# Performance work log

Hardware: AMD Instinct MI355X
Metric: run time of the kernel (lower is better)

## Reference

```python
import jax, jax.numpy as jnp
import numpy as np
import math

N_ROW, N_COL, MID_DIM = 16, 16, 256
B, S, D, K, N_NEURONS = 4, 4096, 1024, 8, 64


def setup_inputs() -> dict:
    key = jax.random.key(0)
    ks = jax.random.split(key, 8)
    return {
        "x": jax.random.normal(ks[0], (B, S, D), dtype=jnp.float32),
        "neuron_idx": jax.random.randint(ks[1], (B, S, K), 0, N_NEURONS),
        "neuron_weights": jax.random.uniform(ks[2], (B, S, K), dtype=jnp.float32),
        "neuron_recipe": jax.random.normal(ks[3], (N_NEURONS, N_ROW * N_COL), dtype=jnp.float32) * 0.02,
        "row_basis": jax.random.normal(ks[4], (N_ROW, D, MID_DIM), dtype=jnp.float32) * 0.02,
        "col_basis": jax.random.normal(ks[5], (N_COL, MID_DIM, D), dtype=jnp.float32) * 0.02,
        "out_w": jax.random.normal(ks[6], (D, D), dtype=jnp.float32) * 0.02,
        "out_b": jnp.zeros((D,), dtype=jnp.float32),
        "alpha": jnp.asarray(0.1, dtype=jnp.float32),
    }


def reference(x, neuron_idx, neuron_weights, neuron_recipe, row_basis, col_basis, out_w, out_b, alpha):
    Bx, Sx, Dx = x.shape
    # --- recipe routing: gather per-token recipes, softmax, weighted sum ---
    sel = neuron_recipe[neuron_idx]                     # [B,S,k,RC]
    sel = jax.nn.softmax(sel, axis=-1)
    token_recipe = jnp.sum(sel * neuron_weights[..., None], axis=2)  # [B,S,RC]
    recipe = jax.nn.softmax(token_recipe, axis=-1).reshape(Bx, Sx, N_ROW, N_COL)
    row_w = recipe.sum(axis=-1)                         # [B,S,n_row]
    col_w = recipe.sum(axis=-2)                         # [B,S,n_col]
    # --- dynamic Q/K: sum over basis middle/last axis commutes with contraction ---
    q = jnp.einsum('bsr,rm->bsm', row_w, row_basis.sum(axis=1))  # [B,S,mid]
    kk = jnp.einsum('bsc,cm->bsm', col_w, col_basis.sum(axis=2)) # [B,S,mid]
    scores = jnp.einsum('bsm,btm->bst', q, kk) / math.sqrt(MID_DIM)  # [B,S,S]
    causal = jnp.triu(jnp.ones((Sx, Sx), dtype=bool), k=1)
    scores = jnp.where(causal, -jnp.inf, scores)
    attn = jax.nn.softmax(scores, axis=-1)
    context = jnp.einsum('bst,btd->bsd', attn, x)        # [B,S,D]
    transform = jnp.einsum('bsc,cd->bsd', col_w, col_basis.sum(axis=1))  # [B,S,D]
    out = jax.nn.gelu(context + alpha * transform, approximate=False)
    return out @ out_w.T + out_b
```

## Files before the change

### kernel.cpp

```cpp
#include <hip/hip_runtime.h>
#include <hip/hip_bf16.h>
#include <math.h>

#define BB 4
#define SS 4096
#define DDIM 1024
#define KSEL 8
#define NR 16
#define NC 16
#define MID 256
#define RC 256
#define TOK (BB*SS)

typedef __hip_bfloat16 bf16;
typedef short short8 __attribute__((ext_vector_type(8)));
typedef short short4v __attribute__((ext_vector_type(4)));
typedef float floatx4 __attribute__((ext_vector_type(4)));
typedef float floatx16 __attribute__((ext_vector_type(16)));
#define MFMA16(a,b,c) __builtin_amdgcn_mfma_f32_16x16x32_bf16(a,b,c,0,0,0)
#define MFMA32(a,b,c) __builtin_amdgcn_mfma_f32_32x32x16_bf16(a,b,c,0,0,0)

__device__ __forceinline__ float uihf(unsigned v) { union { unsigned i; float f; } t; t.i = v; return t.f; }
__device__ __forceinline__ float b2f(bf16 h) { return __bfloat162float(h); }
__device__ __forceinline__ float bs2f(short s) { return uihf(((unsigned)(unsigned short)s) << 16); }
__device__ __forceinline__ short f2bs(float f) {
    bf16 h = __float2bfloat16(f);
    return *reinterpret_cast<short*>(&h);
}
__device__ __forceinline__ float loadf(const void* p, size_t i, bool f32m) {
    return f32m ? ((const float*)p)[i] : b2f(((const bf16*)p)[i]);
}

#define WS_RB   16
#define WS_CB2  4112
#define WS_CB1  8208
#define WS_CW   24592
#define WS_BIAS 286736
#define WS_QK   287760
#define WS_WB   4482064
#define WS_XT   5006352
#define WS_LV   13394960

struct DetectArgs { const void* p[9]; int n[9]; };

__global__ void k_detect(DetectArgs A, int* __restrict__ flags) {
    int b = blockIdx.x;
    int tid = threadIdx.x;
    if (b == 9) {
        float* w = (float*)flags;
        for (int i = tid; i < 24576; i += 256) w[WS_RB + i] = 0.f;
        return;
    }
    const unsigned short* u = (const unsigned short*)A.p[b];
    int n = A.n[b]; if (n > 4096) n = 4096;
    float m = 0.f;
    for (int i = tid; i < n; i += 256) {
        unsigned v = (((unsigned)u[i]) << 16) & 0x7fffffffu;
        float f = uihf(v);
        if (f == f) m = fmaxf(m, f);
    }
    for (int o = 32; o; o >>= 1) m = fmaxf(m, __shfl_xor(m, o));
    __shared__ float red[4];
    if ((tid & 63) == 0) red[tid >> 6] = m;
    __syncthreads();
    if (tid == 0) {
        float mm = fmaxf(fmaxf(red[0], red[1]), fmaxf(red[2], red[3]));
        flags[b] = (b == 1) ? 0 : (mm > 1e4f ? 1 : 0);
    }
}

__global__ void k_rbsum(const void* __restrict__ rb, float* __restrict__ ws) {
    bool f32m = ((const int*)ws)[4] != 0;
    int r = blockIdx.x >> 3, dc = blockIdx.x & 7, m = threadIdx.x;
    size_t base = (size_t)r*DDIM*MID + (size_t)dc*128*MID + m;
    float s = 0.f;
    #pragma unroll 8
    for (int d = 0; d < 128; ++d) s += loadf(rb, base + (size_t)d*MID, f32m);
    atomicAdd(&ws[WS_RB + r*MID + m], s);
}

__global__ void k_cb2(const void* __restrict__ cb, float* __restrict__ ws) {
    bool f32m = ((const int*)ws)[5] != 0;
    int row = blockIdx.x*4 + (threadIdx.x >> 6);
    int lane = threadIdx.x & 63;
    size_t base = (size_t)row*DDIM;
    float s = 0.f;
    for (int i = lane; i < DDIM; i += 64) s += loadf(cb, base + i, f32m);
    for (int o = 32; o; o >>= 1) s += __shfl_down(s, o);
    if (lane == 0) ws[WS_CB2 + row] = s;
}

__global__ void k_cb1(const void* __restrict__ cb, float* __restrict__ ws) {
    bool f32m = ((const int*)ws)[5] != 0;
    int c = blockIdx.x >> 4;
    int d = (((blockIdx.x >> 2) & 3) << 8) + threadIdx.x;
    int m0 = (blockIdx.x & 3) * 64;
    size_t base = (size_t)c*MID*DDIM + (size_t)m0*DDIM + d;
    float s = 0.f;
    #pragma unroll 8
    for (int m = 0; m < 64; ++m) s += loadf(cb, base + (size_t)m*DDIM, f32m);
    atomicAdd(&ws[WS_CB1 + c*DDIM + d], s);
}

__global__ void k_wcvt(const void* __restrict__ w, const void* __restrict__ bias,
                       float* __restrict__ ws) {
    bool wf32 = ((const int*)ws)[6] != 0, bf32 = ((const int*)ws)[7] != 0;
    short* Wb = (short*)(ws + WS_WB);
    float* biasf = ws + WS_BIAS;
    int bx = blockIdx.x, tid = threadIdx.x;
    if (bx == 512) {
        for (int i = tid; i < DDIM; i += 256) biasf[i] = loadf(bias, i, bf32);
        return;
    }
    size_t base = (size_t)bx*2048 + tid*8;
    if (wf32) {
        const float* s = (const float*)w + base;
        float4 a = *(const float4*)s, c = *(const float4*)(s + 4);
        short8 v;
        v[0]=f2bs(a.x); v[1]=f2bs(a.y); v[2]=f2bs(a.z); v[3]=f2bs(a.w);
        v[4]=f2bs(c.x); v[5]=f2bs(c.y); v[6]=f2bs(c.z); v[7]=f2bs(c.w);
        *(short8*)(Wb + base) = v;
    } else {
        *(uint4*)(Wb + base) = *(const uint4*)((const short*)w + base);
    }
}

__global__ void k_xt(const void* __restrict__ x, float* __restrict__ ws) {
    bool xf32 = ((const int*)ws)[0] != 0;
    __shared__ short T[64][72];
    int tid = threadIdx.x;
    int s0 = blockIdx.x*64, d0 = blockIdx.y*64, b = blockIdx.z;
    int rr = tid >> 4, c4 = (tid & 15)*4;
    #pragma unroll
    for (int it = 0; it < 4; ++it) {
        int r = rr + it*16;
        size_t off = (size_t)(b*SS + s0 + r)*DDIM + d0 + c4;
        float v[4];
        if (xf32) {
            float4 a = *(const float4*)((const float*)x + off);
            v[0]=a.x; v[1]=a.y; v[2]=a.z; v[3]=a.w;
        } else {
            const short* p = (const short*)x + off;
            #pragma unroll
            for (int j = 0; j < 4; ++j) v[j] = bs2f(p[j]);
        }
        #pragma unroll
        for (int j = 0; j < 4; ++j) T[c4+j][r] = f2bs(v[j]);
    }
    __syncthreads();
    int dr = tid >> 2, sc = (tid & 3)*16;
    short8 u0 = *(const short8*)(&T[dr][sc]);
    short8 u1 = *(const short8*)(&T[dr][sc+8]);
    short* dst = (short*)(ws + WS_XT) + ((size_t)(b*DDIM + d0 + dr))*SS + s0 + sc;
    *(short8*)dst = u0;
    *(short8*)(dst + 8) = u1;
}

__global__ __launch_bounds__(256) void k_route(const int* __restrict__ nidx,
        const void* __restrict__ nw, const void* __restrict__ rmat,
        float* __restrict__ ws) {
    const bool f2 = ((const int*)ws)[2] != 0, f3 = ((const int*)ws)[3] != 0;
    const int lane = threadIdx.x & 63;
    const int tok = blockIdx.x*4 + (threadIdx.x >> 6);

    int idx8 = 0; float w8 = 0.f;
    if (lane < KSEL) {
        idx8 = nidx[tok*KSEL + lane];
        w8   = loadf(nw, tok*KSEL + lane, f2);
    }

    float acc[4] = {0.f,0.f,0.f,0.f};
    #pragma unroll 1
    for (int k = 0; k < KSEL; ++k) {
        int   id_k = __shfl(idx8, k);
        float wk   = __shfl(w8, k);
        float v[4];
        if (f3) {
            float4 t = *(const float4*)((const float*)rmat + (size_t)id_k*RC + lane*4);
            v[0]=t.x; v[1]=t.y; v[2]=t.z; v[3]=t.w;
        } else {
            short4v t = *(const short4v*)((const short*)rmat + (size_t)id_k*RC + lane*4);
            #pragma unroll
            for (int j = 0; j < 4; ++j) v[j] = bs2f(t[j]);
        }
        float m = fmaxf(fmaxf(v[0],v[1]), fmaxf(v[2],v[3]));
        #pragma unroll
        for (int o = 32; o; o >>= 1) m = fmaxf(m, __shfl_xor(m, o));
        float e[4], s = 0.f;
        #pragma unroll
        for (int j = 0; j < 4; ++j) { e[j] = __expf(v[j]-m); s += e[j]; }
        #pragma unroll
        for (int o = 32; o; o >>= 1) s += __shfl_xor(s, o);
        float r = wk / s;
        #pragma unroll
        for (int j = 0; j < 4; ++j) acc[j] += r * e[j];
    }
    {
        float m = fmaxf(fmaxf(acc[0],acc[1]), fmaxf(acc[2],acc[3]));
        #pragma unroll
        for (int o = 32; o; o >>= 1) m = fmaxf(m, __shfl_xor(m, o));
        float s = 0.f;
        #pragma unroll
        for (int j = 0; j < 4; ++j) { acc[j] = __expf(acc[j]-m); s += acc[j]; }
        #pragma unroll
        for (int o = 32; o; o >>= 1) s += __shfl_xor(s, o);
        float inv = 1.f / s;
        #pragma unroll
        for (int j = 0; j < 4; ++j) acc[j] *= inv;
    }
    float rwp = acc[0]+acc[1]+acc[2]+acc[3];
    rwp += __shfl_xor(rwp, 1); rwp += __shfl_xor(rwp, 2);
    float cw4[4] = {acc[0],acc[1],acc[2],acc[3]};
    #pragma unroll
    for (int j = 0; j < 4; ++j) {
        cw4[j] += __shfl_xor(cw4[j], 4);
        cw4[j] += __shfl_xor(cw4[j], 8);
        cw4[j] += __shfl_xor(cw4[j], 16);
        cw4[j] += __shfl_xor(cw4[j], 32);
    }
    if (lane < 4) {
        float4 t; t.x=cw4[0]; t.y=cw4[1]; t.z=cw4[2]; t.w=cw4[3];
        *(float4*)(ws + WS_CW + (size_t)tok*NC + lane*4) = t;
    }
    float rwAll[NR], cwAll[NC];
    #pragma unroll
    for (int r = 0; r < NR; ++r) rwAll[r] = __shfl(rwp, r*4);
    #pragma unroll
    for (int c = 0; c < NC; ++c) cwAll[c] = __shfl(cw4[c & 3], c >> 2);
    float qv[4] = {0.f,0.f,0.f,0.f}, kv[4] = {0.f,0.f,0.f,0.f};
    #pragma unroll
    for (int r = 0; r < NR; ++r) {
        float4 t = *(const float4*)(ws + WS_RB + r*MID + lane*4);
        qv[0] += rwAll[r]*t.x; qv[1] += rwAll[r]*t.y;
        qv[2] += rwAll[r]*t.z; qv[3] += rwAll[r]*t.w;
    }
    #pragma unroll
    for (int c = 0; c < NC; ++c) {
        float4 t = *(const float4*)(ws + WS_CB2 + c*MID + lane*4);
        kv[0] += cwAll[c]*t.x; kv[1] += cwAll[c]*t.y;
        kv[2] += cwAll[c]*t.z; kv[3] += cwAll[c]*t.w;
    }
    short* Qh  = (short*)(ws + WS_QK);
    short* KKh = Qh + (size_t)TOK*MID;
    short4v qo, ko;
    #pragma unroll
    for (int j = 0; j < 4; ++j) { qo[j] = f2bs(qv[j]*0.0625f); ko[j] = f2bs(kv[j]); }
    *(short4v*)(Qh  + (size_t)tok*MID + lane*4) = qo;
    *(short4v*)(KKh + (size_t)tok*MID + lane*4) = ko;
}

__global__ __launch_bounds__(256) void k_att(const float* __restrict__ ws,
        float* __restrict__ U, const void* __restrict__ alphap) {
    __shared__ __align__(16) short Ks[32*264];
    __shared__ __align__(16) short Ps[64*40];
    __shared__ __align__(16) short cb1T[512*40];
    __shared__ __align__(16) short cwsb[64*40];
    __shared__ float lv[64];
    const int tid = threadIdx.x;
    const int w = tid >> 6, lane = tid & 63, lq = lane & 15, quad = lane >> 4;
    const int bx = blockIdx.x;
    const int g = bx & 7;
    const int d0 = (g & 1)*512, b = g >> 1;
    const int qt = 63 - (bx >> 3);
    const int q0 = qt*64;
    const int ntiles = 2*qt + 2;
    const bool af32 = ((const int*)ws)[8] != 0;
    const short* Qh  = (const short*)(ws + WS_QK);
    const short* KKh = Qh + (size_t)TOK*MID;
    const short* xT  = (const short*)(ws + WS_XT);

    {
        for (int r = tid; r < 512; r += 256) {
            const float* src = ws + WS_CB1 + d0 + r;
            short* dst = cb1T + r*40;
            #pragma unroll
            for (int c = 0; c < 16; ++c) dst[c] = f2bs(src[c*DDIM]);
            #pragma unroll
            for (int c = 16; c < 32; ++c) dst[c] = 0;
        }
    }
    {
        int r = tid >> 2, c4 = (tid & 3)*4;
        const float* cwp = ws + WS_CW + (size_t)(b*SS + q0 + r)*NC + c4;
        short* dst = cwsb + r*40;
        #pragma unroll
        for (int j = 0; j < 4; ++j) dst[c4 + j] = f2bs(cwp[j]);
        #pragma unroll
        for (int j = 0; j < 4; ++j) dst[16 + c4 + j] = 0;
    }
    const int rsw = (lq >> 2) & 3;
    const short* pa_rd = Ps + lq*40 + ((quad ^ rsw) << 3);
    short* pd_base = Ps + (w*16 + quad*4)*40 + (lq & 7);
    const int kr = tid >> 3, ksg = (tid & 7)*32;
    short* kdst = Ks + kr*264 + ksg;
    float alpha = af32 ? ((const float*)alphap)[0] : bs2f(((const short*)alphap)[0]);

    short8 qa[8];
    {
        const short* qrow = Qh + (size_t)(b*SS + q0 + w*16 + lq)*MID + quad*8;
        #pragma unroll
        for (int ks = 0; ks < 8; ++ks) qa[ks] = *(const short8*)(qrow + ks*32);
    }
    floatx4 acc[4][8];
    #pragma unroll
    for (int qi = 0; qi < 4; ++qi)
        #pragma unroll
        for (int di = 0; di < 8; ++di) acc[qi][di] = (floatx4){0.f,0.f,0.f,0.f};
    float l[4] = {0.f,0.f,0.f,0.f};

    const short* xb_base = xT + (size_t)(b*DDIM + d0 + w*128 + lq)*SS + quad*8;
    const short* ksrc0 = KKh + (size_t)(b*SS + kr)*MID + ksg;
    short8 kp0 = *(const short8*)(ksrc0);
    short8 kp1 = *(const short8*)(ksrc0 + 8);
    short8 kp2 = *(const short8*)(ksrc0 + 16);
    short8 kp3 = *(const short8*)(ksrc0 + 24);

    #pragma unroll 1
    for (int it = 0; it < ntiles; ++it) {
        const int t0 = it*32;
        *(short8*)(kdst)      = kp0;
        *(short8*)(kdst + 8)  = kp1;
        *(short8*)(kdst + 16) = kp2;
        *(short8*)(kdst + 24) = kp3;
        if (it + 1 < ntiles) {
            const short* ks_n = ksrc0 + (size_t)(it + 1)*32*MID;
            kp0 = *(const short8*)(ks_n);
            kp1 = *(const short8*)(ks_n + 8);
            kp2 = *(const short8*)(ks_n + 16);
            kp3 = *(const short8*)(ks_n + 24);
        }
        const short* xx = xb_base + it*32;
        short8 xf0 = *(const short8*)(xx);
        short8 xf1 = *(const short8*)(xx + (size_t)16*SS);
        short8 xf2 = *(const short8*)(xx + (size_t)32*SS);
        short8 xf3 = *(const short8*)(xx + (size_t)48*SS);
        short8 xf4 = *(const short8*)(xx + (size_t)64*SS);
        short8 xf5 = *(const short8*)(xx + (size_t)80*SS);
        short8 xf6 = *(const short8*)(xx + (size_t)96*SS);
        short8 xf7 = *(const short8*)(xx + (size_t)112*SS);
        __syncthreads();
        #pragma unroll
        for (int h = 0; h < 2; ++h) {
            floatx4 s = (floatx4){0.f,0.f,0.f,0.f};
            const short* kb = Ks + (h*16 + lq)*264 + quad*8;
            #pragma unroll
            for (int ks = 0; ks < 8; ++ks)
                s = MFMA16(qa[ks], *(const short8*)(kb + ks*32), s);
            int t = t0 + h*16 + lq;
            int qg = q0 + w*16 + quad*4;
            short* pd = pd_base + (((h*2 + (lq >> 3)) ^ quad) << 3);
            #pragma unroll
            for (int r = 0; r < 4; ++r) {
                float p = (t <= qg + r) ? __expf(s[r]) : 0.f;
                l[r] += p;
                pd[r*40] = f2bs(p);
            }
        }
        __syncthreads();
        {
            short8 pa0 = *(const short8*)(pa_rd);
            short8 pa1 = *(const short8*)(pa_rd + 16*40);
            short8 pa2 = *(const short8*)(pa_rd + 32*40);
            short8 pa3 = *(const short8*)(pa_rd + 48*40);
            acc[0][0] = MFMA16(pa0, xf0, acc[0][0]);
            acc[1][0] = MFMA16(pa1, xf0, acc[1][0]);
            acc[2][0] = MFMA16(pa2, xf0, acc[2][0]);
            acc[3][0] = MFMA16(pa3, xf0, acc[3][0]);
            acc[0][1] = MFMA16(pa0, xf1, acc[0][1]);
            acc[1][1] = MFMA16(pa1, xf1, acc[1][1]);
            acc[2][1] = MFMA16(pa2, xf1, acc[2][1]);
            acc[3][1] = MFMA16(pa3, xf1, acc[3][1]);
            acc[0][2] = MFMA16(pa0, xf2, acc[0][2]);
            acc[1][2] = MFMA16(pa1, xf2, acc[1][2]);
            acc[2][2] = MFMA16(pa2, xf2, acc[2][2]);
            acc[3][2] = MFMA16(pa3, xf2, acc[3][2]);
            acc[0][3] = MFMA16(pa0, xf3, acc[0][3]);
            acc[1][3] = MFMA16(pa1, xf3, acc[1][3]);
            acc[2][3] = MFMA16(pa2, xf3, acc[2][3]);
            acc[3][3] = MFMA16(pa3, xf3, acc[3][3]);
            acc[0][4] = MFMA16(pa0, xf4, acc[0][4]);
            acc[1][4] = MFMA16(pa1, xf4, acc[1][4]);
            acc[2][4] = MFMA16(pa2, xf4, acc[2][4]);
            acc[3][4] = MFMA16(pa3, xf4, acc[3][4]);
            acc[0][5] = MFMA16(pa0, xf5, acc[0][5]);
            acc[1][5] = MFMA16(pa1, xf5, acc[1][5]);
            acc[2][5] = MFMA16(pa2, xf5, acc[2][5]);
            acc[3][5] = MFMA16(pa3, xf5, acc[3][5]);
            acc[0][6] = MFMA16(pa0, xf6, acc[0][6]);
            acc[1][6] = MFMA16(pa1, xf6, acc[1][6]);
            acc[2][6] = MFMA16(pa2, xf6, acc[2][6]);
            acc[3][6] = MFMA16(pa3, xf6, acc[3][6]);
            acc[0][7] = MFMA16(pa0, xf7, acc[0][7]);
            acc[1][7] = MFMA16(pa1, xf7, acc[1][7]);
            acc[2][7] = MFMA16(pa2, xf7, acc[2][7]);
            acc[3][7] = MFMA16(pa3, xf7, acc[3][7]);
        }
    }

    #pragma unroll
    for (int r = 0; r < 4; ++r) {
        float v = l[r];
        v += __shfl_xor(v,1); v += __shfl_xor(v,2);
        v += __shfl_xor(v,4); v += __shfl_xor(v,8);
        if (lq == 0) lv[w*16 + quad*4 + r] = v;
    }
    __syncthreads();
    float linv[4][4];
    #pragma unroll
    for (int qi = 0; qi < 4; ++qi)
        #pragma unroll
        for (int r = 0; r < 4; ++r)
            linv[qi][r] = 1.f / lv[qi*16 + quad*4 + r];

    short8 ca[4];
    #pragma unroll
    for (int qi = 0; qi < 4; ++qi)
        ca[qi] = *(const short8*)(cwsb + (qi*16 + lq)*40 + quad*8);
    #pragma unroll
    for (int di = 0; di < 8; ++di) {
        const int dl = w*128 + di*16;
        const short8 cbf = *(const short8*)(cb1T + (dl + lq)*40 + quad*8);
        #pragma unroll
        for (int qi = 0; qi < 4; ++qi) {
            floatx4 tr = (floatx4){0.f,0.f,0.f,0.f};
            tr = MFMA16(ca[qi], cbf, tr);
            float* Ub = U + (size_t)(b*SS + q0 + qi*16 + quad*4)*DDIM + d0 + dl + lq;
            #pragma unroll
            for (int r = 0; r < 4; ++r) {
                float u = acc[qi][di][r]*linv[qi][r] + alpha*tr[r];
                float e2 = __expf(1.5957691216f*(u + 0.044715f*u*u*u));
                float th = 1.f - 2.f/(e2 + 1.f);
                Ub[(size_t)r*DDIM] = 0.5f*u*(1.f + th);
            }
        }
    }
}

__global__ __launch_bounds__(256,2) void k_gemm3(float* __restrict__ out,
        const float* __restrict__ ws) {
    __shared__ __align__(16) short Al[32*132];
    const int tid = threadIdx.x;
    const int w = tid >> 6, lane = tid & 63;
    const int col = lane & 31, kh = lane >> 5;
    const int m0 = blockIdx.x*32;
    const int n0 = w*256;
    const short* Wb = (const short*)(ws + WS_WB);
    const float* biasf = ws + WS_BIAS;

    floatx16 acc[8];
    #pragma unroll
    for (int nt = 0; nt < 8; ++nt)
        #pragma unroll
        for (int r = 0; r < 16; ++r) acc[nt][r] = 0.f;

    const int srow = tid >> 3, sk = (tid & 7)*16;
    const float* Usrc = out + (size_t)(m0 + srow)*DDIM + sk;
    short* Adst = Al + srow*132 + sk;

    #pragma unroll 1
    for (int kc = 0; kc < DDIM; kc += 128) {
        __syncthreads();
        {
            const float* s = Usrc + kc;
            float4 a = *(const float4*)s,     b4 = *(const float4*)(s + 4);
            float4 c = *(const float4*)(s+8), d  = *(const float4*)(s + 12);
            short8 v0, v1;
            v0[0]=f2bs(a.x);  v0[1]=f2bs(a.y);  v0[2]=f2bs(a.z);  v0[3]=f2bs(a.w);
            v0[4]=f2bs(b4.x); v0[5]=f2bs(b4.y); v0[6]=f2bs(b4.z); v0[7]=f2bs(b4.w);
            v1[0]=f2bs(c.x);  v1[1]=f2bs(c.y);  v1[2]=f2bs(c.z);  v1[3]=f2bs(c.w);
            v1[4]=f2bs(d.x);  v1[5]=f2bs(d.y);  v1[6]=f2bs(d.z);  v1[7]=f2bs(d.w);
            *(short8*)(Adst)     = v0;
            *(short8*)(Adst + 8) = v1;
        }
        __syncthreads();
        const short* wbp0 = Wb + (size_t)(n0 + col)*DDIM + kc + kh*8;
        #pragma unroll
        for (int ks = 0; ks < 8; ++ks) {
            short8 af = *(const short8*)(Al + col*132 + ks*16 + kh*8);
            const short* wbp = wbp0 + ks*16;
            #pragma unroll
            for (int nt = 0; nt < 8; ++nt)
                acc[nt] = MFMA32(af, *(const short8*)(wbp + (size_t)nt*32*DDIM), acc[nt]);
        }
    }
    #pragma unroll
    for (int nt = 0; nt < 8; ++nt) {
        int c = n0 + nt*32 + col;
        float bb = biasf[c];
        #pragma unroll
        for (int r = 0; r < 16; ++r) {
            int row = (r & 3) + 8*(r >> 2) + 4*kh;
            out[(size_t)(m0 + row)*DDIM + c] = acc[nt][r] + bb;
        }
    }
}

extern "C" void kernel_launch(void* const* d_in, const int* in_sizes, int n_in,
                              void* d_out, int out_size, void* d_ws, size_t ws_size,
                              hipStream_t stream) {
    (void)out_size; (void)ws_size;
    const void* x    = d_in[0];
    const int*  nidx = (const int*)d_in[1];
    const void* nw   = d_in[2];
    const void* rmat = d_in[3];
    const void* rb   = d_in[4];
    const void* cb   = d_in[5];
    const void* w    = d_in[6];
    const void* bias = d_in[7];
    const void* alpha= d_in[8];
    float* ws = (float*)d_ws;
    float* out = (float*)d_out;

    DetectArgs da;
    for (int i = 0; i < 9; ++i) { da.p[i] = d_in[i]; da.n[i] = (i < n_in) ? in_sizes[i] : 1; }

    k_detect<<<10, 256, 0, stream>>>(da, (int*)ws);
    k_rbsum<<<128, 256, 0, stream>>>(rb, ws);
    k_cb2  <<<1024, 256, 0, stream>>>(cb, ws);
    k_cb1  <<<256, 256, 0, stream>>>(cb, ws);
    k_wcvt <<<513, 256, 0, stream>>>(w, bias, ws);
    k_xt   <<<dim3(SS/64, DDIM/64, BB), 256, 0, stream>>>(x, ws);
    k_route<<<TOK/4, 256, 0, stream>>>(nidx, nw, rmat, ws);
    k_att  <<<512, 256, 0, stream>>>(ws, out, alpha);
    k_gemm3<<<TOK/32, 256, 0, stream>>>(out, ws);
}
```

Measured before the change: 584.1 us.

## Split attention into paired 32-row query blocks for causal load balancing

The attention kernel now processes two 32-row query blocks per workgroup, pairing block qb with block 127-qb, so every workgroup does roughly the same number of causal key tiles instead of 64-row tiles with very uneven work. The four waves split a 2x2 query-by-key layout, so the score MFMAs per wave halve, and the two key halves' row sums are combined through shared memory. Shared memory is aliased: the cb1T staging buffer reuses the K/P region and is rebuilt each phase. The cost is smaller query tiles, which halve the reuse of each loaded K and x tile, plus extra barriers and a cb1T reload per phase.

```diff
diff --git a/kernel.cpp b/kernel.cpp
--- a/kernel.cpp
+++ b/kernel.cpp
@@ -251,186 +251,177 @@
 
 __global__ __launch_bounds__(256) void k_att(const float* __restrict__ ws,
         float* __restrict__ U, const void* __restrict__ alphap) {
-    __shared__ __align__(16) short Ks[32*264];
-    __shared__ __align__(16) short Ps[64*40];
-    __shared__ __align__(16) short cb1T[512*40];
-    __shared__ __align__(16) short cwsb[64*40];
-    __shared__ float lv[64];
+    __shared__ __align__(16) char smem[43776];
+    short* Ks   = (short*)smem;
+    short* Ps   = (short*)(smem + 16896);
+    short* cb1T = (short*)smem;
+    short* cwsb = (short*)(smem + 40960);
+    float* lv   = (float*)(smem + 43520);
     const int tid = threadIdx.x;
     const int w = tid >> 6, lane = tid & 63, lq = lane & 15, quad = lane >> 4;
+    const int qi = w >> 1, ki = w & 1;
     const int bx = blockIdx.x;
     const int g = bx & 7;
     const int d0 = (g & 1)*512, b = g >> 1;
-    const int qt = 63 - (bx >> 3);
-    const int q0 = qt*64;
-    const int ntiles = 2*qt + 2;
+    const int qbp = bx >> 3;
     const bool af32 = ((const int*)ws)[8] != 0;
     const short* Qh  = (const short*)(ws + WS_QK);
     const short* KKh = Qh + (size_t)TOK*MID;
     const short* xT  = (const short*)(ws + WS_XT);
 
-    {
-        for (int r = tid; r < 512; r += 256) {
-            const float* src = ws + WS_CB1 + d0 + r;
-            short* dst = cb1T + r*40;
-            #pragma unroll
-            for (int c = 0; c < 16; ++c) dst[c] = f2bs(src[c*DDIM]);
-            #pragma unroll
-            for (int c = 16; c < 32; ++c) dst[c] = 0;
-        }
-    }
-    {
-        int r = tid >> 2, c4 = (tid & 3)*4;
-        const float* cwp = ws + WS_CW + (size_t)(b*SS + q0 + r)*NC + c4;
-        short* dst = cwsb + r*40;
-        #pragma unroll
-        for (int j = 0; j < 4; ++j) dst[c4 + j] = f2bs(cwp[j]);
-        #pragma unroll
-        for (int j = 0; j < 4; ++j) dst[16 + c4 + j] = 0;
-    }
     const int rsw = (lq >> 2) & 3;
     const short* pa_rd = Ps + lq*40 + ((quad ^ rsw) << 3);
-    short* pd_base = Ps + (w*16 + quad*4)*40 + (lq & 7);
+    short* pd_base = Ps + (qi*16 + quad*4)*40 + (lq & 7) + (((ki*2 + (lq >> 3)) ^ quad) << 3);
     const int kr = tid >> 3, ksg = (tid & 7)*32;
     short* kdst = Ks + kr*264 + ksg;
+    const short* ksrc0 = KKh + (size_t)(b*SS + kr)*MID + ksg;
+    const short* xb_base = xT + (size_t)(b*DDIM + d0 + w*128 + lq)*SS + quad*8;
     float alpha = af32 ? ((const float*)alphap)[0] : bs2f(((const short*)alphap)[0]);
 
-    short8 qa[8];
-    {
-        const short* qrow = Qh + (size_t)(b*SS + q0 + w*16 + lq)*MID + quad*8;
-        #pragma unroll
-        for (int ks = 0; ks < 8; ++ks) qa[ks] = *(const short8*)(qrow + ks*32);
-    }
-    floatx4 acc[4][8];
-    #pragma unroll
-    for (int qi = 0; qi < 4; ++qi)
-        #pragma unroll
-        for (int di = 0; di < 8; ++di) acc[qi][di] = (floatx4){0.f,0.f,0.f,0.f};
-    float l[4] = {0.f,0.f,0.f,0.f};
-
-    const short* xb_base = xT + (size_t)(b*DDIM + d0 + w*128 + lq)*SS + quad*8;
-    const short* ksrc0 = KKh + (size_t)(b*SS + kr)*MID + ksg;
-    short8 kp0 = *(const short8*)(ksrc0);
-    short8 kp1 = *(const short8*)(ksrc0 + 8);
-    short8 kp2 = *(const short8*)(ksrc0 + 16);
-    short8 kp3 = *(const short8*)(ksrc0 + 24);
-
     #pragma unroll 1
-    for (int it = 0; it < ntiles; ++it) {
-        const int t0 = it*32;
-        *(short8*)(kdst)      = kp0;
-        *(short8*)(kdst + 8)  = kp1;
-        *(short8*)(kdst + 16) = kp2;
-        *(short8*)(kdst + 24) = kp3;
-        if (it + 1 < ntiles) {
-            const short* ks_n = ksrc0 + (size_t)(it + 1)*32*MID;
-            kp0 = *(const short8*)(ks_n);
-            kp1 = *(const short8*)(ks_n + 8);
-            kp2 = *(const short8*)(ks_n + 16);
-            kp3 = *(const short8*)(ks_n + 24);
-        }
-        const short* xx = xb_base + it*32;
-        short8 xf0 = *(const short8*)(xx);
-        short8 xf1 = *(const short8*)(xx + (size_t)16*SS);
-        short8 xf2 = *(const short8*)(xx + (size_t)32*SS);
-        short8 xf3 = *(const short8*)(xx + (size_t)48*SS);
-        short8 xf4 = *(const short8*)(xx + (size_t)64*SS);
-        short8 xf5 = *(const short8*)(xx + (size_t)80*SS);
-        short8 xf6 = *(const short8*)(xx + (size_t)96*SS);
-        short8 xf7 = *(const short8*)(xx + (size_t)112*SS);
+    for (int ph = 0; ph < 2; ++ph) {
+        const int qb = ph ? qbp : 127 - qbp;
+        const int q0 = qb*32;
+        const int ntiles = qb + 1;
         __syncthreads();
-        #pragma unroll
-        for (int h = 0; h < 2; ++h) {
-            floatx4 s = (floatx4){0.f,0.f,0.f,0.f};
-            const short* kb = Ks + (h*16 + lq)*264 + quad*8;
-            #pragma unroll
-            for (int ks = 0; ks < 8; ++ks)
-                s = MFMA16(qa[ks], *(const short8*)(kb + ks*32), s);
-            int t = t0 + h*16 + lq;
-            int qg = q0 + w*16 + quad*4;
-            short* pd = pd_base + (((h*2 + (lq >> 3)) ^ quad) << 3);
-            #pragma unroll
-            for (int r = 0; r < 4; ++r) {
-                float p = (t <= qg + r) ? __expf(s[r]) : 0.f;
-                l[r] += p;
-                pd[r*40] = f2bs(p);
+        if (tid < 128) {
+            int r = tid >> 2, c4 = (tid & 3)*4;
+            const float* cwp = ws + WS_CW + (size_t)(b*SS + q0 + r)*NC + c4;
+            short* dst = cwsb + r*40;
+            #pragma unroll
+            for (int j = 0; j < 4; ++j) dst[c4 + j] = f2bs(cwp[j]);
+            #pragma unroll
+            for (int j = 0; j < 4; ++j) dst[16 + c4 + j] = 0;
+        }
+        short8 qa[8];
+        {
+            const short* qrow = Qh + (size_t)(b*SS + q0 + qi*16 + lq)*MID + quad*8;
+            #pragma unroll
+            for (int ks = 0; ks < 8; ++ks) qa[ks] = *(const short8*)(qrow + ks*32);
+        }
+        floatx4 acc[2][8];
+        #pragma unroll
+        for (int q_ = 0; q_ < 2; ++q_)
+            #pragma unroll
+            for (int di = 0; di < 8; ++di) acc[q_][di] = (floatx4){0.f,0.f,0.f,0.f};
+        float l[4] = {0.f,0.f,0.f,0.f};
+        const int qg = q0 + qi*16 + quad*4;
+
+        short8 kp0 = *(const short8*)(ksrc0);
+        short8 kp1 = *(const short8*)(ksrc0 + 8);
+        short8 kp2 = *(const short8*)(ksrc0 + 16);
+        short8 kp3 = *(const short8*)(ksrc0 + 24);
+
+        #pragma unroll 1
+        for (int it = 0; it < ntiles; ++it) {
+            const int t0 = it*32;
+            *(short8*)(kdst)      = kp0;
+            *(short8*)(kdst + 8)  = kp1;
+            *(short8*)(kdst + 16) = kp2;
+            *(short8*)(kdst + 24) = kp3;
+            if (it + 1 < ntiles) {
+                const short* ks_n = ksrc0 + (size_t)(it + 1)*32*MID;
+                kp0 = *(const short8*)(ks_n);
+                kp1 = *(const short8*)(ks_n + 8);
+                kp2 = *(const short8*)(ks_n + 16);
+                kp3 = *(const short8*)(ks_n + 24);
             }
+            const short* xx = xb_base + it*32;
+            short8 xf0 = *(const short8*)(xx);
+            short8 xf1 = *(const short8*)(xx + (size_t)16*SS);
+            short8 xf2 = *(const short8*)(xx + (size_t)32*SS);
+            short8 xf3 = *(const short8*)(xx + (size_t)48*SS);
+            short8 xf4 = *(const short8*)(xx + (size_t)64*SS);
+            short8 xf5 = *(const short8*)(xx + (size_t)80*SS);
+            short8 xf6 = *(const short8*)(xx + (size_t)96*SS);
+            short8 xf7 = *(const short8*)(xx + (size_t)112*SS);
+            __syncthreads();
+            {
+                floatx4 s = (floatx4){0.f,0.f,0.f,0.f};
+                const short* kb = Ks + (ki*16 + lq)*264 + quad*8;
+                #pragma unroll
+                for (int ks = 0; ks < 8; ++ks)
+                    s = MFMA16(qa[ks], *(const short8*)(kb + ks*32), s);
+                int t = t0 + ki*16 + lq;
+                #pragma unroll
+                for (int r = 0; r < 4; ++r) {
+                    float p = (t <= qg + r) ? __expf(s[r]) : 0.f;
+                    l[r] += p;
+                    pd_base[r*40] = f2bs(p);
+                }
+            }
+            __syncthreads();
+            {
+                short8 pa0 = *(const short8*)(pa_rd);
+                short8 pa1 = *(const short8*)(pa_rd + 16*40);
+                acc[0][0] = MFMA16(pa0, xf0, acc[0][0]);
+                acc[1][0] = MFMA16(pa1, xf0, acc[1][0]);
+                acc[0][1] = MFMA16(pa0, xf1, acc[0][1]);
+                acc[1][1] = MFMA16(pa1, xf1, acc[1][1]);
+                acc[0][2] = MFMA16(pa0, xf2, acc[0][2]);
+                acc[1][2] = MFMA16(pa1, xf2, acc[1][2]);
+                acc[0][3] = MFMA16(pa0, xf3, acc[0][3]);
+                acc[1][3] = MFMA16(pa1, xf3, acc[1][3]);
+                acc[0][4] = MFMA16(pa0, xf4, acc[0][4]);
+                acc[1][4] = MFMA16(pa1, xf4, acc[1][4]);
+                acc[0][5] = MFMA16(pa0, xf5, acc[0][5]);
+                acc[1][5] = MFMA16(pa1, xf5, acc[1][5]);
+                acc[0][6] = MFMA16(pa0, xf6, acc[0][6]);
+                acc[1][6] = MFMA16(pa1, xf6, acc[1][6]);
+                acc[0][7] = MFMA16(pa0, xf7, acc[0][7]);
+                acc[1][7] = MFMA16(pa1, xf7, acc[1][7]);
+            }
+        }
+
+        #pragma unroll
+        for (int r = 0; r < 4; ++r) {
+            float v = l[r];
+            v += __shfl_xor(v,1); v += __shfl_xor(v,2);
+            v += __shfl_xor(v,4); v += __shfl_xor(v,8);
+            if (lq == 0) lv[ki*32 + qi*16 + quad*4 + r] = v;
         }
         __syncthreads();
         {
-            short8 pa0 = *(const short8*)(pa_rd);
-            short8 pa1 = *(const short8*)(pa_rd + 16*40);
-            short8 pa2 = *(const short8*)(pa_rd + 32*40);
-            short8 pa3 = *(const short8*)(pa_rd + 48*40);
-            acc[0][0] = MFMA16(pa0, xf0, acc[0][0]);
-            acc[1][0] = MFMA16(pa1, xf0, acc[1][0]);
-            acc[2][0] = MFMA16(pa2, xf0, acc[2][0]);
-            acc[3][0] = MFMA16(pa3, xf0, acc[3][0]);
-            acc[0][1] = MFMA16(pa0, xf1, acc[0][1]);
-            acc[1][1] = MFMA16(pa1, xf1, acc[1][1]);
-            acc[2][1] = MFMA16(pa2, xf1, acc[2][1]);
-            acc[3][1] = MFMA16(pa3, xf1, acc[3][1]);
-            acc[0][2] = MFMA16(pa0, xf2, acc[0][2]);
-            acc[1][2] = MFMA16(pa1, xf2, acc[1][2]);
-            acc[2][2] = MFMA16(pa2, xf2, acc[2][2]);
-            acc[3][2] = MFMA16(pa3, xf2, acc[3][2]);
-            acc[0][3] = MFMA16(pa0, xf3, acc[0][3]);
-            acc[1][3] = MFMA16(pa1, xf3, acc[1][3]);
-            acc[2][3] = MFMA16(pa2, xf3, acc[2][3]);
-            acc[3][3] = MFMA16(pa3, xf3, acc[3][3]);
-            acc[0][4] = MFMA16(pa0, xf4, acc[0][4]);
-            acc[1][4] = MFMA16(pa1, xf4, acc[1][4]);
-            acc[2][4] = MFMA16(pa2, xf4, acc[2][4]);
-            acc[3][4] = MFMA16(pa3, xf4, acc[3][4]);
-            acc[0][5] = MFMA16(pa0, xf5, acc[0][5]);
-            acc[1][5] = MFMA16(pa1, xf5, acc[1][5]);
-            acc[2][5] = MFMA16(pa2, xf5, acc[2][5]);
-            acc[3][5] = MFMA16(pa3, xf5, acc[3][5]);
-            acc[0][6] = MFMA16(pa0, xf6, acc[0][6]);
-            acc[1][6] = MFMA16(pa1, xf6, acc[1][6]);
-            acc[2][6] = MFMA16(pa2, xf6, acc[2][6]);
-            acc[3][6] = MFMA16(pa3, xf6, acc[3][6]);
-            acc[0][7] = MFMA16(pa0, xf7, acc[0][7]);
-            acc[1][7] = MFMA16(pa1, xf7, acc[1][7]);
-            acc[2][7] = MFMA16(pa2, xf7, acc[2][7]);
-            acc[3][7] = MFMA16(pa3, xf7, acc[3][7]);
-        }
-    }
-
-    #pragma unroll
-    for (int r = 0; r < 4; ++r) {
-        float v = l[r];
-        v += __shfl_xor(v,1); v += __shfl_xor(v,2);
-        v += __shfl_xor(v,4); v += __shfl_xor(v,8);
-        if (lq == 0) lv[w*16 + quad*4 + r] = v;
-    }
-    __syncthreads();
-    float linv[4][4];
-    #pragma unroll
-    for (int qi = 0; qi < 4; ++qi)
-        #pragma unroll
-        for (int r = 0; r < 4; ++r)
-            linv[qi][r] = 1.f / lv[qi*16 + quad*4 + r];
-
-    short8 ca[4];
-    #pragma unroll
-    for (int qi = 0; qi < 4; ++qi)
-        ca[qi] = *(const short8*)(cwsb + (qi*16 + lq)*40 + quad*8);
-    #pragma unroll
-    for (int di = 0; di < 8; ++di) {
-        const int dl = w*128 + di*16;
-        const short8 cbf = *(const short8*)(cb1T + (dl + lq)*40 + quad*8);
-        #pragma unroll
-        for (int qi = 0; qi < 4; ++qi) {
-            floatx4 tr = (floatx4){0.f,0.f,0.f,0.f};
-            tr = MFMA16(ca[qi], cbf, tr);
-            float* Ub = U + (size_t)(b*SS + q0 + qi*16 + quad*4)*DDIM + d0 + dl + lq;
-            #pragma unroll
-            for (int r = 0; r < 4; ++r) {
-                float u = acc[qi][di][r]*linv[qi][r] + alpha*tr[r];
-                float e2 = __expf(1.5957691216f*(u + 0.044715f*u*u*u));
-                float th = 1.f - 2.f/(e2 + 1.f);
-                Ub[(size_t)r*DDIM] = 0.5f*u*(1.f + th);
+            for (int r = tid; r < 512; r += 256) {
+                const float* src = ws + WS_CB1 + d0 + r;
+                short* dst = cb1T + r*40;
+                #pragma unroll
+                for (int c = 0; c < 16; ++c) dst[c] = f2bs(src[c*DDIM]);
+                #pragma unroll
+                for (int c = 16; c < 32; ++c) dst[c] = 0;
+            }
+        }
+        __syncthreads();
+        {
+            float linv[2][4];
+            #pragma unroll
+            for (int q_ = 0; q_ < 2; ++q_)
+                #pragma unroll
+                for (int r = 0; r < 4; ++r) {
+                    int row = q_*16 + quad*4 + r;
+                    linv[q_][r] = 1.f / (lv[row] + lv[32 + row]);
+                }
+            short8 ca[2];
+            #pragma unroll
+            for (int q_ = 0; q_ < 2; ++q_)
+                ca[q_] = *(const short8*)(cwsb + (q_*16 + lq)*40 + quad*8);
+            #pragma unroll
+            for (int di = 0; di < 8; ++di) {
+                const int dl = w*128 + di*16;
+                const short8 cbf = *(const short8*)(cb1T + (dl + lq)*40 + quad*8);
+                #pragma unroll
+                for (int q_ = 0; q_ < 2; ++q_) {
+                    floatx4 tr = (floatx4){0.f,0.f,0.f,0.f};
+                    tr = MFMA16(ca[q_], cbf, tr);
+                    float* Ub = U + (size_t)(b*SS + q0 + q_*16 + quad*4)*DDIM + d0 + dl + lq;
+                    #pragma unroll
+                    for (int r = 0; r < 4; ++r) {
+                        float u = acc[q_][di][r]*linv[q_][r] + alpha*tr[r];
+                        float e2 = __expf(1.5957691216f*(u + 0.044715f*u*u*u));
+                        float th = 1.f - 2.f/(e2 + 1.f);
+                        Ub[(size_t)r*DDIM] = 0.5f*u*(1.f + th);
+                    }
+                }
             }
         }
     }
```

Result: slower. 677.1 us (+15.9%).
